# Performance work log

Hardware: AMD Instinct MI355X
Metric: run time of the kernel (lower is better)

## Reference

```python
import jax, jax.numpy as jnp
import numpy as np

DIM = 512
HEADS = 8
DIM_HEAD = 64
INNER = HEADS * DIM_HEAD  # 512
LN_EPS = 1e-5


def setup_inputs() -> dict:
    key = jax.random.key(0)
    ks = jax.random.split(key, 6)
    b, n = 2, 2048
    x = jax.random.normal(ks[0], (b, n, DIM), dtype=jnp.float32)
    # to_qkv: Linear(dim, inner*3, bias=False); torch weight is [out,in], apply as x @ W.T
    w_qkv = jax.random.normal(ks[1], (3 * INNER, DIM), dtype=jnp.float32) * (DIM ** -0.5)
    reattn_w = jax.random.normal(ks[2], (HEADS, HEADS), dtype=jnp.float32)
    ln_g = jnp.ones((HEADS,), dtype=jnp.float32)
    ln_b = jnp.zeros((HEADS,), dtype=jnp.float32)
    w_out = jax.random.normal(ks[3], (DIM, INNER), dtype=jnp.float32) * (INNER ** -0.5)
    b_out = jnp.zeros((DIM,), dtype=jnp.float32)
    return {"x": x, "w_qkv": w_qkv, "reattn_w": reattn_w,
            "ln_g": ln_g, "ln_b": ln_b, "w_out": w_out, "b_out": b_out}


def reference(x, w_qkv, reattn_w, ln_g, ln_b, w_out, b_out):
    b, n, _ = x.shape
    scale = DIM_HEAD ** -0.5
    qkv = x @ w_qkv.T  # [b, n, 3*inner]
    q, k, v = jnp.split(qkv, 3, axis=-1)
    # b n (h d) -> b h n d
    split_heads = lambda t: t.reshape(b, n, HEADS, DIM_HEAD).transpose(0, 2, 1, 3)
    q, k, v = split_heads(q), split_heads(k), split_heads(v)
    dots = jnp.einsum('bhid,bhjd->bhij', q, k) * scale
    attn = jax.nn.softmax(dots, axis=-1)
    # re-attention: cross-head mixing then LayerNorm over head dim
    attn = jnp.einsum('bhij,hg->bgij', attn, reattn_w)
    a = attn.transpose(0, 2, 3, 1)  # b i j h
    mu = jnp.mean(a, axis=-1, keepdims=True)
    var = jnp.mean((a - mu) ** 2, axis=-1, keepdims=True)
    a = (a - mu) * jax.lax.rsqrt(var + LN_EPS) * ln_g + ln_b
    attn = a.transpose(0, 3, 1, 2)  # b h i j
    out = jnp.einsum('bhij,bhjd->bhid', attn, v)
    out = out.transpose(0, 2, 1, 3).reshape(b, n, INNER)
    out = out @ w_out.T + b_out  # dropout p=0 -> identity
    return out
```

## Files before the change

kernel.cpp:

```cpp
#include <hip/hip_runtime.h>
#include <hip/hip_bf16.h>


typedef __attribute__((ext_vector_type(8))) short bfx8;
typedef __attribute__((ext_vector_type(4))) float f32x4;
typedef unsigned short u16;
typedef unsigned int u32;

#define QSCALE 0.18033688011112042f

static __device__ inline u16 f2bf(float f) {
  union { float f; unsigned u; } cv; cv.f = f;
  unsigned u = cv.u;
  u += 0x7fffu + ((u >> 16) & 1u);
  return (u16)(u >> 16);
}
static __device__ inline u32 cvtpk(float lo, float hi) {
  u32 d; asm("v_cvt_pk_bf16_f32 %0, %1, %2" : "=v"(d) : "v"(lo), "v"(hi)); return d;
}
static __device__ inline float fexp2(float x) {
  float r; asm("v_exp_f32 %0, %1" : "=v"(r) : "v"(x)); return r;
}
static __device__ inline float flog2(float x) {
  float r; asm("v_log_f32 %0, %1" : "=v"(r) : "v"(x)); return r;
}
static __device__ inline uint4 pk8(const float* p) {
  float4 a = *(const float4*)p, b = *(const float4*)(p + 4);
  return make_uint4(cvtpk(a.x, a.y), cvtpk(a.z, a.w), cvtpk(b.x, b.y), cvtpk(b.z, b.w));
}

__global__ __launch_bounds__(256) void gemm_qkv(
    const float* __restrict__ A, const float* __restrict__ B,
    u16* __restrict__ qb, u16* __restrict__ kb, u16* __restrict__ vtb) {
  __shared__ u16 As[128 * 32];
  __shared__ u16 Bs[128 * 32];
  const int t = threadIdx.x, lane = t & 63;
  const int wm = (t >> 6) >> 1, wn = (t >> 6) & 1;
  const int m0 = blockIdx.y * 128, n0 = blockIdx.x * 128;
  const int li = lane & 15, lg = lane >> 4;
  const int rowA = t >> 2, kb8 = (t & 3) * 8;
  f32x4 acc[4][4] = {};
  for (int k0 = 0; k0 < 512; k0 += 32) {
    __syncthreads();
    *(uint4*)&As[rowA * 32 + kb8]        = pk8(&A[(size_t)(m0 + rowA) * 512 + k0 + kb8]);
    *(uint4*)&As[(rowA + 64) * 32 + kb8] = pk8(&A[(size_t)(m0 + rowA + 64) * 512 + k0 + kb8]);
    *(uint4*)&Bs[rowA * 32 + kb8]        = pk8(&B[(size_t)(n0 + rowA) * 512 + k0 + kb8]);
    *(uint4*)&Bs[(rowA + 64) * 32 + kb8] = pk8(&B[(size_t)(n0 + rowA + 64) * 512 + k0 + kb8]);
    __syncthreads();
    bfx8 af[4], bf_[4];
#pragma unroll
    for (int mi = 0; mi < 4; mi++)
      af[mi] = *(const bfx8*)&As[(wm * 64 + mi * 16 + li) * 32 + lg * 8];
#pragma unroll
    for (int ni = 0; ni < 4; ni++)
      bf_[ni] = *(const bfx8*)&Bs[(wn * 64 + ni * 16 + li) * 32 + lg * 8];
#pragma unroll
    for (int mi = 0; mi < 4; mi++)
#pragma unroll
      for (int ni = 0; ni < 4; ni++)
        acc[mi][ni] = __builtin_amdgcn_mfma_f32_16x16x32_bf16(af[mi], bf_[ni], acc[mi][ni], 0, 0, 0);
  }
#pragma unroll
  for (int mi = 0; mi < 4; mi++) {
#pragma unroll
    for (int ni = 0; ni < 4; ni++) {
      const int nc  = n0 + wn * 64 + ni * 16 + li;
      const int mrb = m0 + wm * 64 + mi * 16 + lg * 4;
      const int part = nc >> 9, within = nc & 511;
      const int h = within >> 6, d = within & 63;
      const int bb = mrb >> 11, ii = mrb & 2047;
      if (part == 0) {
#pragma unroll
        for (int r = 0; r < 4; r++)
          qb[(((size_t)bb * 8 + h) * 2048 + ii + r) * 64 + d] = f2bf(acc[mi][ni][r] * QSCALE);
      } else if (part == 1) {
#pragma unroll
        for (int r = 0; r < 4; r++)
          kb[(((size_t)bb * 8 + h) * 2048 + ii + r) * 64 + d] = f2bf(acc[mi][ni][r]);
      } else {
        ushort4 u;
        u.x = f2bf(acc[mi][ni][0]); u.y = f2bf(acc[mi][ni][1]);
        u.z = f2bf(acc[mi][ni][2]); u.w = f2bf(acc[mi][ni][3]);
        *(ushort4*)&vtb[(((size_t)bb * 8 + h) * 64 + d) * 2048 + ii] = u;
      }
    }
  }
}

__global__ __launch_bounds__(256) void passA(
    const u16* __restrict__ qb, const u16* __restrict__ kb,
    float2* __restrict__ statp) {
  const int t = threadIdx.x, lane = t & 63, w = t >> 6;
  const int bh = blockIdx.y, js = blockIdx.z;
  const int i0 = blockIdx.x * 64 + w * 16;
  const int li = lane & 15, lg = lane >> 4;
  const u16* Qh = qb + ((size_t)bh * 2048 + i0 + li) * 64;
  const u16* Kb = kb + (size_t)bh * 2048 * 64;
  const bfx8 q0 = *(const bfx8*)&Qh[lg * 8];
  const bfx8 q1 = *(const bfx8*)&Qh[32 + lg * 8];
  float m = -1e30f, l = 0.f;
  const int jbeg = js * 512, jend = jbeg + 512;
  for (int j0 = jbeg; j0 < jend; j0 += 32) {
    const u16* KhA = Kb + (size_t)(j0 + li) * 64;
    const u16* KhB = KhA + 16 * 64;
    bfx8 a0 = *(const bfx8*)&KhA[lg * 8];
    bfx8 a1 = *(const bfx8*)&KhA[32 + lg * 8];
    bfx8 b0 = *(const bfx8*)&KhB[lg * 8];
    bfx8 b1 = *(const bfx8*)&KhB[32 + lg * 8];
    __builtin_amdgcn_sched_barrier(0);
    f32x4 sa = {0.f, 0.f, 0.f, 0.f}, sb = {0.f, 0.f, 0.f, 0.f};
    sa = __builtin_amdgcn_mfma_f32_16x16x32_bf16(a0, q0, sa, 0, 0, 0);
    sa = __builtin_amdgcn_mfma_f32_16x16x32_bf16(a1, q1, sa, 0, 0, 0);
    sb = __builtin_amdgcn_mfma_f32_16x16x32_bf16(b0, q0, sb, 0, 0, 0);
    sb = __builtin_amdgcn_mfma_f32_16x16x32_bf16(b1, q1, sb, 0, 0, 0);
    float mt = fmaxf(fmaxf(fmaxf(sa[0], sa[1]), fmaxf(sa[2], sa[3])),
                     fmaxf(fmaxf(sb[0], sb[1]), fmaxf(sb[2], sb[3])));
    float mn = fmaxf(m, mt);
    float es = (fexp2(sa[0] - mn) + fexp2(sa[1] - mn)) + (fexp2(sa[2] - mn) + fexp2(sa[3] - mn))
             + (fexp2(sb[0] - mn) + fexp2(sb[1] - mn)) + (fexp2(sb[2] - mn) + fexp2(sb[3] - mn));
    l = fmaf(l, fexp2(m - mn), es);
    m = mn;
  }
  for (int off = 16; off < 64; off <<= 1) {
    float mo = __shfl_xor(m, off, 64);
    float lo = __shfl_xor(l, off, 64);
    float mn = fmaxf(m, mo);
    l = l * fexp2(m - mn) + lo * fexp2(mo - mn);
    m = mn;
  }
  if (lane < 16) statp[(size_t)js * 32768 + (size_t)bh * 2048 + i0 + li] = make_float2(m, l);
}

__global__ __launch_bounds__(512) void kFused(
    const u16* __restrict__ qb, const u16* __restrict__ kb,
    const u16* __restrict__ vtb, const float2* __restrict__ statp,
    const float* __restrict__ Wmix, const float* __restrict__ lng,
    const float* __restrict__ lnb, float* __restrict__ innerF) {
  __shared__ __align__(16) u16 Spk[64 * 512];
  __shared__ __align__(16) u16 A2h[8 * 64 * 72];
  __shared__ float stMs[64 * 8];
  const int t = threadIdx.x, lane = t & 63, w = t >> 6;
  const int li = lane & 15, lg = lane >> 4;
  const int ig = blockIdx.x * 64, b = blockIdx.y, j0 = blockIdx.z * 512;

  float wm_[8][8], lng_[8], lnb_[8];
#pragma unroll
  for (int h = 0; h < 8; h++)
#pragma unroll
    for (int g = 0; g < 8; g++) wm_[h][g] = Wmix[h * 8 + g];
#pragma unroll
  for (int g = 0; g < 8; g++) { lng_[g] = lng[g]; lnb_[g] = lnb[g]; }

  {
    const int i = t >> 3, h = t & 7;
    const size_t idx = ((size_t)(b * 8 + h)) * 2048 + ig + i;
    float m = -1e30f, l = 0.f;
#pragma unroll
    for (int z = 0; z < 4; z++) {
      const float2 a = statp[(size_t)z * 32768 + idx];
      const float mn = fmaxf(m, a.x);
      l = l * fexp2(m - mn) + a.y * fexp2(a.x - mn);
      m = mn;
    }
    stMs[i * 8 + h] = m + flog2(l);
  }

  bfx8 qf[4][2];
#pragma unroll
  for (int ii = 0; ii < 4; ii++)
#pragma unroll
    for (int ks = 0; ks < 2; ks++)
      qf[ii][ks] = *(const bfx8*)&qb[(((size_t)(b * 8 + w)) * 2048 + ig + ii * 16 + li) * 64
                                     + ks * 32 + lg * 8];
  __syncthreads();
  float stMp[4];
#pragma unroll
  for (int ii = 0; ii < 4; ii++) stMp[ii] = stMs[(ii * 16 + li) * 8 + w];

  f32x4 pacc[4][4] = {};
  const int mixI = t >> 3, mixJ8 = (t & 7) * 8;
  const int mixSwz = (mixI & 7) << 3;

  bfx8 kf[4][2];
#pragma unroll
  for (int ji = 0; ji < 4; ji++)
#pragma unroll
    for (int ks = 0; ks < 2; ks++)
      kf[ji][ks] = *(const bfx8*)&kb[(((size_t)(b * 8 + w)) * 2048 + j0 + ji * 16 + li) * 64
                                     + ks * 32 + lg * 8];

  for (int jt = j0; jt < j0 + 512; jt += 64) {
    bfx8 vf0[4], vf1[4];
#pragma unroll
    for (int dt = 0; dt < 4; dt++) {
      vf0[dt] = *(const bfx8*)&vtb[(((size_t)(b * 8 + w)) * 64 + dt * 16 + li) * 2048
                                   + jt + lg * 8];
      vf1[dt] = *(const bfx8*)&vtb[(((size_t)(b * 8 + w)) * 64 + dt * 16 + li) * 2048
                                   + jt + 32 + lg * 8];
    }
    __builtin_amdgcn_sched_barrier(0);
#pragma unroll
    for (int ii = 0; ii < 4; ii++) {
      f32x4 s[4] = {};
#pragma unroll
      for (int ji = 0; ji < 4; ji++) {
        s[ji] = __builtin_amdgcn_mfma_f32_16x16x32_bf16(kf[ji][0], qf[ii][0], s[ji], 0, 0, 0);
        s[ji] = __builtin_amdgcn_mfma_f32_16x16x32_bf16(kf[ji][1], qf[ii][1], s[ji], 0, 0, 0);
      }
      const int i = ii * 16 + li;
      const int swzI = (i & 7) << 3;
#pragma unroll
      for (int ji = 0; ji < 4; ji++) {
        const float p0 = fexp2(s[ji][0] - stMp[ii]);
        const float p1 = fexp2(s[ji][1] - stMp[ii]);
        const float p2 = fexp2(s[ji][2] - stMp[ii]);
        const float p3 = fexp2(s[ji][3] - stMp[ii]);
        const int x = (ji * 16 + lg * 4) ^ swzI;
        *(uint2*)&Spk[i * 512 + w * 64 + x] = make_uint2(cvtpk(p0, p1), cvtpk(p2, p3));
      }
    }
    {
      const int jn = (jt + 64 < j0 + 512) ? jt + 64 : j0;
#pragma unroll
      for (int ji = 0; ji < 4; ji++)
#pragma unroll
        for (int ks = 0; ks < 2; ks++)
          kf[ji][ks] = *(const bfx8*)&kb[(((size_t)(b * 8 + w)) * 2048 + jn + ji * 16 + li) * 64
                                         + ks * 32 + lg * 8];
      __builtin_amdgcn_sched_barrier(0);
    }
    __syncthreads();
    {
      u32 ogw[8][4];
      float tmp[8];
#pragma unroll
      for (int hf = 0; hf < 2; hf++) {
        float p[8][4];
#pragma unroll
        for (int h = 0; h < 8; h++) {
          const int x4 = (mixJ8 + hf * 4) ^ mixSwz;
          const uint2 v = *(const uint2*)&Spk[mixI * 512 + h * 64 + x4];
          union { u32 u; float f; } c0, c1, c2, c3;
          c0.u = v.x << 16; c1.u = v.x & 0xffff0000u;
          c2.u = v.y << 16; c3.u = v.y & 0xffff0000u;
          p[h][0] = c0.f; p[h][1] = c1.f; p[h][2] = c2.f; p[h][3] = c3.f;
        }
#pragma unroll
        for (int e = 0; e < 4; e++) {
          float a_[8]; float sum = 0.f, sumsq = 0.f;
#pragma unroll
          for (int g = 0; g < 8; g++) {
            float acc = 0.f;
#pragma unroll
            for (int h = 0; h < 8; h++) acc = fmaf(p[h][e], wm_[h][g], acc);
            a_[g] = acc; sum += acc; sumsq = fmaf(acc, acc, sumsq);
          }
          const float mu = sum * 0.125f;
          const float var = fmaf(sumsq, 0.125f, -mu * mu);
          const float rs = rsqrtf(var + 1e-5f);
#pragma unroll
          for (int g = 0; g < 8; g++) {
            const float av = fmaf((a_[g] - mu) * rs, lng_[g], lnb_[g]);
            if (e & 1) ogw[g][hf * 2 + (e >> 1)] = cvtpk(tmp[g], av);
            else       tmp[g] = av;
          }
        }
      }
#pragma unroll
      for (int g = 0; g < 8; g++)
        *(uint4*)&A2h[g * 4608 + mixI * 72 + (mixJ8 ^ mixSwz)] =
            make_uint4(ogw[g][0], ogw[g][1], ogw[g][2], ogw[g][3]);
    }
    __syncthreads();
    __builtin_amdgcn_s_setprio(1);
#pragma unroll
    for (int iSub = 0; iSub < 4; iSub++) {
      const bfx8 af0 = *(const bfx8*)&A2h[w * 4608 + (iSub * 16 + li) * 72
                                          + ((lg * 8) ^ ((li & 7) << 3))];
#pragma unroll
      for (int dt = 0; dt < 4; dt++)
        pacc[iSub][dt] = __builtin_amdgcn_mfma_f32_16x16x32_bf16(af0, vf0[dt], pacc[iSub][dt], 0, 0, 0);
    }
#pragma unroll
    for (int iSub = 0; iSub < 4; iSub++) {
      const bfx8 af1 = *(const bfx8*)&A2h[w * 4608 + (iSub * 16 + li) * 72
                                          + ((32 + lg * 8) ^ ((li & 7) << 3))];
#pragma unroll
      for (int dt = 0; dt < 4; dt++)
        pacc[iSub][dt] = __builtin_amdgcn_mfma_f32_16x16x32_bf16(af1, vf1[dt], pacc[iSub][dt], 0, 0, 0);
    }
    __builtin_amdgcn_s_setprio(0);
    __syncthreads();
  }
#pragma unroll
  for (int iSub = 0; iSub < 4; iSub++)
#pragma unroll
    for (int dt = 0; dt < 4; dt++)
#pragma unroll
      for (int r = 0; r < 4; r++)
        atomicAdd(&innerF[((size_t)b * 2048 + ig + iSub * 16 + lg * 4 + r) * 512
                          + w * 64 + dt * 16 + li],
                  pacc[iSub][dt][r]);
}

__global__ __launch_bounds__(256) void convertInner(
    const float* __restrict__ inF, u16* __restrict__ outB) {
  int e = (blockIdx.x * 256 + threadIdx.x) * 4;
  float4 v = *(const float4*)&inF[e];
  ushort4 o; o.x = f2bf(v.x); o.y = f2bf(v.y); o.z = f2bf(v.z); o.w = f2bf(v.w);
  *(ushort4*)&outB[e] = o;
}

__global__ __launch_bounds__(256) void gemm_out(
    const u16* __restrict__ A, const float* __restrict__ B,
    float* __restrict__ outf, const float* __restrict__ bias) {
  __shared__ u16 As[128 * 32];
  __shared__ u16 Bs[128 * 32];
  const int t = threadIdx.x, lane = t & 63;
  const int wm = (t >> 6) >> 1, wn = (t >> 6) & 1;
  const int m0 = blockIdx.y * 128, n0 = blockIdx.x * 128;
  const int li = lane & 15, lg = lane >> 4;
  const int rowA = t >> 2, kb8 = (t & 3) * 8;
  f32x4 acc[4][4] = {};
  for (int k0 = 0; k0 < 512; k0 += 32) {
    __syncthreads();
    *(bfx8*)&As[rowA * 32 + kb8]        = *(const bfx8*)&A[(size_t)(m0 + rowA) * 512 + k0 + kb8];
    *(bfx8*)&As[(rowA + 64) * 32 + kb8] = *(const bfx8*)&A[(size_t)(m0 + rowA + 64) * 512 + k0 + kb8];
    *(uint4*)&Bs[rowA * 32 + kb8]        = pk8(&B[(size_t)(n0 + rowA) * 512 + k0 + kb8]);
    *(uint4*)&Bs[(rowA + 64) * 32 + kb8] = pk8(&B[(size_t)(n0 + rowA + 64) * 512 + k0 + kb8]);
    __syncthreads();
    bfx8 af[4], bf_[4];
#pragma unroll
    for (int mi = 0; mi < 4; mi++)
      af[mi] = *(const bfx8*)&As[(wm * 64 + mi * 16 + li) * 32 + lg * 8];
#pragma unroll
    for (int ni = 0; ni < 4; ni++)
      bf_[ni] = *(const bfx8*)&Bs[(wn * 64 + ni * 16 + li) * 32 + lg * 8];
#pragma unroll
    for (int mi = 0; mi < 4; mi++)
#pragma unroll
      for (int ni = 0; ni < 4; ni++)
        acc[mi][ni] = __builtin_amdgcn_mfma_f32_16x16x32_bf16(af[mi], bf_[ni], acc[mi][ni], 0, 0, 0);
  }
#pragma unroll
  for (int mi = 0; mi < 4; mi++) {
#pragma unroll
    for (int ni = 0; ni < 4; ni++) {
      const int nc  = n0 + wn * 64 + ni * 16 + li;
      const int mrb = m0 + wm * 64 + mi * 16 + lg * 4;
      const float bv = bias[nc];
#pragma unroll
      for (int r = 0; r < 4; r++)
        outf[(size_t)(mrb + r) * 512 + nc] = acc[mi][ni][r] + bv;
    }
  }
}

extern "C" void kernel_launch(void* const* d_in, const int* in_sizes, int n_in,
                              void* d_out, int out_size, void* d_ws, size_t ws_size,
                              hipStream_t stream) {
  const float* x      = (const float*)d_in[0];
  const float* w_qkv  = (const float*)d_in[1];
  const float* reattn = (const float*)d_in[2];
  const float* ln_g   = (const float*)d_in[3];
  const float* ln_b   = (const float*)d_in[4];
  const float* w_out  = (const float*)d_in[5];
  const float* b_out  = (const float*)d_in[6];
  float* out = (float*)d_out;
  char* ws = (char*)d_ws;
  float*  innerF= (float*)(ws + 0);
  u16*    qbf   = (u16*)(ws + 8388608);
  u16*    kbf   = (u16*)(ws + 12582912);
  u16*    vtb   = (u16*)(ws + 16777216);
  float2* statp = (float2*)(ws + 20971520);
  u16*    innerB= (u16*)(ws + 8388608);

  gemm_qkv<<<dim3(12, 32), 256, 0, stream>>>(x, w_qkv, qbf, kbf, vtb);
  hipMemsetAsync(innerF, 0, 8388608, stream);
  passA<<<dim3(32, 16, 4), 256, 0, stream>>>(qbf, kbf, statp);
  kFused<<<dim3(32, 2, 4), 512, 0, stream>>>(qbf, kbf, vtb, statp, reattn, ln_g, ln_b, innerF);
  convertInner<<<2048, 256, 0, stream>>>(innerF, innerB);
  gemm_out<<<dim3(4, 32), 256, 0, stream>>>(innerB, w_out, out, b_out);
}
```

Measured before the change: 197.7 us.

## Swizzle block order for XCD locality, fuse inner conversion into output GEMM, reorder loads

Remaps the 1D block index in gemm_qkv, passA and gemm_out so consecutive blocks on the same XCD share input tiles, aiming for better L2 reuse. Removes the convertInner kernel by having gemm_out read the fp32 accumulator and pack it to bf16 while loading tiles, which saves a launch and a round trip of the intermediate. In kFused, the V fragment loads move after the barrier, and the mixing stage now reads its bf16 probabilities with one 16-byte LDS load per head instead of two 8-byte loads. In exchange, gemm_out reads twice as many bytes for A, and the V loads now sit closer to their use, so less of their latency is hidden.

```diff
diff --git a/kernel.cpp b/kernel.cpp
--- a/kernel.cpp
+++ b/kernel.cpp
@@ -34,9 +34,11 @@
     u16* __restrict__ qb, u16* __restrict__ kb, u16* __restrict__ vtb) {
   __shared__ u16 As[128 * 32];
   __shared__ u16 Bs[128 * 32];
+  const int bid = blockIdx.x;
+  const int swzb = (bid & 7) * 48 + (bid >> 3);
+  const int n0 = (swzb % 12) * 128, m0 = (swzb / 12) * 128;
   const int t = threadIdx.x, lane = t & 63;
   const int wm = (t >> 6) >> 1, wn = (t >> 6) & 1;
-  const int m0 = blockIdx.y * 128, n0 = blockIdx.x * 128;
   const int li = lane & 15, lg = lane >> 4;
   const int rowA = t >> 2, kb8 = (t & 3) * 8;
   f32x4 acc[4][4] = {};
@@ -90,9 +92,11 @@
 __global__ __launch_bounds__(256) void passA(
     const u16* __restrict__ qb, const u16* __restrict__ kb,
     float2* __restrict__ statp) {
+  const int bid = blockIdx.x;
+  const int swzb = (bid & 7) * 256 + (bid >> 3);
+  const int bx = swzb & 31, bh = (swzb >> 5) & 15, js = swzb >> 9;
   const int t = threadIdx.x, lane = t & 63, w = t >> 6;
-  const int bh = blockIdx.y, js = blockIdx.z;
-  const int i0 = blockIdx.x * 64 + w * 16;
+  const int i0 = bx * 64 + w * 16;
   const int li = lane & 15, lg = lane >> 4;
   const u16* Qh = qb + ((size_t)bh * 2048 + i0 + li) * 64;
   const u16* Kb = kb + (size_t)bh * 2048 * 64;
@@ -190,15 +194,6 @@
                                      + ks * 32 + lg * 8];
 
   for (int jt = j0; jt < j0 + 512; jt += 64) {
-    bfx8 vf0[4], vf1[4];
-#pragma unroll
-    for (int dt = 0; dt < 4; dt++) {
-      vf0[dt] = *(const bfx8*)&vtb[(((size_t)(b * 8 + w)) * 64 + dt * 16 + li) * 2048
-                                   + jt + lg * 8];
-      vf1[dt] = *(const bfx8*)&vtb[(((size_t)(b * 8 + w)) * 64 + dt * 16 + li) * 2048
-                                   + jt + 32 + lg * 8];
-    }
-    __builtin_amdgcn_sched_barrier(0);
 #pragma unroll
     for (int ii = 0; ii < 4; ii++) {
       f32x4 s[4] = {};
@@ -219,6 +214,15 @@
         *(uint2*)&Spk[i * 512 + w * 64 + x] = make_uint2(cvtpk(p0, p1), cvtpk(p2, p3));
       }
     }
+    __syncthreads();
+    bfx8 vf0[4], vf1[4];
+#pragma unroll
+    for (int dt = 0; dt < 4; dt++) {
+      vf0[dt] = *(const bfx8*)&vtb[(((size_t)(b * 8 + w)) * 64 + dt * 16 + li) * 2048
+                                   + jt + lg * 8];
+      vf1[dt] = *(const bfx8*)&vtb[(((size_t)(b * 8 + w)) * 64 + dt * 16 + li) * 2048
+                                   + jt + 32 + lg * 8];
+    }
     {
       const int jn = (jt + 64 < j0 + 512) ? jt + 64 : j0;
 #pragma unroll
@@ -227,10 +231,13 @@
         for (int ks = 0; ks < 2; ks++)
           kf[ji][ks] = *(const bfx8*)&kb[(((size_t)(b * 8 + w)) * 2048 + jn + ji * 16 + li) * 64
                                          + ks * 32 + lg * 8];
-      __builtin_amdgcn_sched_barrier(0);
-    }
-    __syncthreads();
+    }
+    __builtin_amdgcn_sched_barrier(0);
     {
+      uint4 sv[8];
+#pragma unroll
+      for (int h = 0; h < 8; h++)
+        sv[h] = *(const uint4*)&Spk[mixI * 512 + h * 64 + (mixJ8 ^ mixSwz)];
       u32 ogw[8][4];
       float tmp[8];
 #pragma unroll
@@ -238,11 +245,11 @@
         float p[8][4];
 #pragma unroll
         for (int h = 0; h < 8; h++) {
-          const int x4 = (mixJ8 + hf * 4) ^ mixSwz;
-          const uint2 v = *(const uint2*)&Spk[mixI * 512 + h * 64 + x4];
+          const u32 va = hf ? sv[h].z : sv[h].x;
+          const u32 vb = hf ? sv[h].w : sv[h].y;
           union { u32 u; float f; } c0, c1, c2, c3;
-          c0.u = v.x << 16; c1.u = v.x & 0xffff0000u;
-          c2.u = v.y << 16; c3.u = v.y & 0xffff0000u;
+          c0.u = va << 16; c1.u = va & 0xffff0000u;
+          c2.u = vb << 16; c3.u = vb & 0xffff0000u;
           p[h][0] = c0.f; p[h][1] = c1.f; p[h][2] = c2.f; p[h][3] = c3.f;
         }
 #pragma unroll
@@ -303,29 +310,23 @@
                   pacc[iSub][dt][r]);
 }
 
-__global__ __launch_bounds__(256) void convertInner(
-    const float* __restrict__ inF, u16* __restrict__ outB) {
-  int e = (blockIdx.x * 256 + threadIdx.x) * 4;
-  float4 v = *(const float4*)&inF[e];
-  ushort4 o; o.x = f2bf(v.x); o.y = f2bf(v.y); o.z = f2bf(v.z); o.w = f2bf(v.w);
-  *(ushort4*)&outB[e] = o;
-}
-
 __global__ __launch_bounds__(256) void gemm_out(
-    const u16* __restrict__ A, const float* __restrict__ B,
+    const float* __restrict__ A, const float* __restrict__ B,
     float* __restrict__ outf, const float* __restrict__ bias) {
   __shared__ u16 As[128 * 32];
   __shared__ u16 Bs[128 * 32];
+  const int bid = blockIdx.x;
+  const int swzb = (bid & 7) * 16 + (bid >> 3);
+  const int n0 = (swzb & 3) * 128, m0 = (swzb >> 2) * 128;
   const int t = threadIdx.x, lane = t & 63;
   const int wm = (t >> 6) >> 1, wn = (t >> 6) & 1;
-  const int m0 = blockIdx.y * 128, n0 = blockIdx.x * 128;
   const int li = lane & 15, lg = lane >> 4;
   const int rowA = t >> 2, kb8 = (t & 3) * 8;
   f32x4 acc[4][4] = {};
   for (int k0 = 0; k0 < 512; k0 += 32) {
     __syncthreads();
-    *(bfx8*)&As[rowA * 32 + kb8]        = *(const bfx8*)&A[(size_t)(m0 + rowA) * 512 + k0 + kb8];
-    *(bfx8*)&As[(rowA + 64) * 32 + kb8] = *(const bfx8*)&A[(size_t)(m0 + rowA + 64) * 512 + k0 + kb8];
+    *(uint4*)&As[rowA * 32 + kb8]        = pk8(&A[(size_t)(m0 + rowA) * 512 + k0 + kb8]);
+    *(uint4*)&As[(rowA + 64) * 32 + kb8] = pk8(&A[(size_t)(m0 + rowA + 64) * 512 + k0 + kb8]);
     *(uint4*)&Bs[rowA * 32 + kb8]        = pk8(&B[(size_t)(n0 + rowA) * 512 + k0 + kb8]);
     *(uint4*)&Bs[(rowA + 64) * 32 + kb8] = pk8(&B[(size_t)(n0 + rowA + 64) * 512 + k0 + kb8]);
     __syncthreads();
@@ -373,12 +374,10 @@
   u16*    kbf   = (u16*)(ws + 12582912);
   u16*    vtb   = (u16*)(ws + 16777216);
   float2* statp = (float2*)(ws + 20971520);
-  u16*    innerB= (u16*)(ws + 8388608);
-
-  gemm_qkv<<<dim3(12, 32), 256, 0, stream>>>(x, w_qkv, qbf, kbf, vtb);
+
+  gemm_qkv<<<384, 256, 0, stream>>>(x, w_qkv, qbf, kbf, vtb);
   hipMemsetAsync(innerF, 0, 8388608, stream);
-  passA<<<dim3(32, 16, 4), 256, 0, stream>>>(qbf, kbf, statp);
+  passA<<<2048, 256, 0, stream>>>(qbf, kbf, statp);
   kFused<<<dim3(32, 2, 4), 512, 0, stream>>>(qbf, kbf, vtb, statp, reattn, ln_g, ln_b, innerF);
-  convertInner<<<2048, 256, 0, stream>>>(innerF, innerB);
-  gemm_out<<<dim3(4, 32), 256, 0, stream>>>(innerB, w_out, out, b_out);
-}
+  gemm_out<<<128, 256, 0, stream>>>(innerF, w_out, out, b_out);
+}
```

Measured after the change: 191.4 us. 3.2% less time.
